# Kernel tuning notes

Hardware: AMD Instinct MI355X
Metric: run time of the kernel (lower is better)

Reference implementation:

```python
import jax, jax.numpy as jnp
import numpy as np

BATCH = 2048
N = 2 * BATCH
TEMP = 0.5
BN_EPS = 1e-5
COS_EPS = 1e-8

# Precompute (constant) flat indices of the negative entries: all (i,j) with
# j != i and j != i +- BATCH. Each row has exactly N-2 negatives.
_mask = np.ones((N, N), dtype=bool)
np.fill_diagonal(_mask, False)
for _i in range(BATCH):
    _mask[_i, BATCH + _i] = False
    _mask[BATCH + _i, _i] = False
NEG_IDX = np.nonzero(_mask.reshape(-1))[0]  # (N*(N-2),)


def _projector(h, W1, gamma, beta, W2, b2):
    # Linear (no bias) -> BatchNorm1d (training-mode batch stats) -> ReLU -> Linear
    x = h @ W1.T                                   # (B, latent)
    mu = jnp.mean(x, axis=0)
    var = jnp.mean(jnp.square(x - mu), axis=0)     # biased var, as torch BN
    x = (x - mu) * jax.lax.rsqrt(var + BN_EPS) * gamma + beta
    x = jax.nn.relu(x)
    return x @ W2.T + b2                           # (B, proj)


def setup_inputs() -> dict:
    key = jax.random.key(0)
    ks = jax.random.split(key, 4)
    latent, proj = 2048, 256
    return {
        "h_i": jax.random.normal(ks[0], (BATCH, latent), jnp.float32),
        "h_j": jax.random.normal(ks[1], (BATCH, latent), jnp.float32),
        "W1": jax.random.normal(ks[2], (latent, latent), jnp.float32) / np.sqrt(latent),
        "gamma": jnp.ones((latent,), jnp.float32),
        "beta": jnp.zeros((latent,), jnp.float32),
        "W2": jax.random.normal(ks[3], (proj, latent), jnp.float32) / np.sqrt(latent),
        "b2": jnp.zeros((proj,), jnp.float32),
    }


def reference(h_i, h_j, W1, gamma, beta, W2, b2):
    z_i = _projector(h_i, W1, gamma, beta, W2, b2)
    z_j = _projector(h_j, W1, gamma, beta, W2, b2)
    z = jnp.concatenate([z_i, z_j], axis=0)                      # (N, proj)
    # cosine similarity: normalize once, then a single GEMM
    zn = z / jnp.maximum(jnp.linalg.norm(z, axis=1, keepdims=True), COS_EPS)
    sim = (zn @ zn.T) / TEMP                                     # (N, N)
    sim_i_j = jnp.diagonal(sim, offset=BATCH)                    # (BATCH,)
    sim_j_i = jnp.diagonal(sim, offset=-BATCH)                   # (BATCH,)
    positives = jnp.concatenate([sim_i_j, sim_j_i])[:, None]     # (N, 1)
    negatives = sim.reshape(-1)[NEG_IDX].reshape(N, N - 2)       # (N, N-2)
    logits = jnp.concatenate([positives, negatives], axis=1)     # (N, N-1)
    # cross-entropy with label 0 for every row, reduction='sum', then / N
    loss = jnp.sum(jax.nn.logsumexp(logits, axis=1) - logits[:, 0]) / N
    return loss
```

## Files before the change

### kernel.cpp

```cpp
#include <hip/hip_runtime.h>
#include <hip/hip_fp8.h>
#include <math.h>

#define BATCH   2048
#define NROWS   4096
#define LATENT  2048
#define PROJ    256
#define TEMP_INV 2.0f
#define BN_EPS  1e-5f
#define COS_EPS 1e-8f
#define W1SCALE 32.0f
#define W1INV   (1.0f / 32.0f)

typedef __bf16 bf16x8 __attribute__((ext_vector_type(8)));
typedef float  f32x4  __attribute__((ext_vector_type(4)));
typedef long   i64;

__device__ __forceinline__ unsigned short f2bf(float f) {
    union { float f; unsigned int u; } c; c.f = f;
    return (unsigned short)((c.u + 0x7FFFu + ((c.u >> 16) & 1u)) >> 16);
}
__device__ __forceinline__ float bf2f(unsigned short h) {
    union { unsigned int u; float f; } c; c.u = ((unsigned int)h) << 16;
    return c.f;
}
__device__ __forceinline__ unsigned char f2fp8(float f) {
    __hip_fp8_e4m3 t(f);
    return (unsigned char)t.__x;
}

__device__ __forceinline__ void gl_lds16(const void* g, void* l) {
    __builtin_amdgcn_global_load_lds(
        (const __attribute__((address_space(1))) void*)g,
        (__attribute__((address_space(3))) void*)l, 16, 0, 0);
}

__device__ __forceinline__ int swz(int R, int lk) {
    return R * 32 + ((lk ^ ((R >> 1) & 3)) << 3);
}
__device__ __forceinline__ int mix8(int R) {
    return (R & 7) ^ ((R >> 1) & 4);
}

#define G1 1048576
#define G2 2097152
#define G3 3145728
#define G4 3276800
__global__ __launch_bounds__(256) void cvt_all_kernel(
    const float* __restrict__ h_i, const float* __restrict__ h_j,
    const float* __restrict__ W1,  const float* __restrict__ W2,
    unsigned char* __restrict__ Hq, unsigned char* __restrict__ W1q,
    unsigned short* __restrict__ W2b)
{
    int i = blockIdx.x * 256 + threadIdx.x;
    if (i >= G4) return;
    if (i < G2) {
        const float* src = (i < G1) ? h_i : h_j;
        int off = (i < G1) ? i : i - G1;
        float4 v = reinterpret_cast<const float4*>(src)[off];
        uchar4 o;
        o.x = f2fp8(v.x); o.y = f2fp8(v.y); o.z = f2fp8(v.z); o.w = f2fp8(v.w);
        reinterpret_cast<uchar4*>(Hq)[i] = o;
    } else if (i < G3) {
        int off = i - G2;
        float4 v = reinterpret_cast<const float4*>(W1)[off];
        uchar4 o;
        o.x = f2fp8(v.x * W1SCALE); o.y = f2fp8(v.y * W1SCALE);
        o.z = f2fp8(v.z * W1SCALE); o.w = f2fp8(v.w * W1SCALE);
        reinterpret_cast<uchar4*>(W1q)[off] = o;
    } else {
        int off = i - G3;
        float4 v = reinterpret_cast<const float4*>(W2)[off];
        ushort4 o;
        o.x = f2bf(v.x); o.y = f2bf(v.y); o.z = f2bf(v.z); o.w = f2bf(v.w);
        reinterpret_cast<ushort4*>(W2b)[off] = o;
    }
}

template<int KSTRIDE, int KLEN, int WM, int WN>
__device__ __forceinline__ void mfma_loop(
    const unsigned short* __restrict__ Ab,
    const unsigned short* __restrict__ Bb,
    unsigned short* As, unsigned short* Bs,
    f32x4 acc[WM][WN], int tid)
{
    constexpr int BM = WM * 32;
    constexpr int BN = WN * 32;
    const int wid = tid >> 6, lane = tid & 63;
    const int mblk = (wid >> 1) * (WM * 16);
    const int nblk = (wid & 1) * (WN * 16);
    const int lr = lane & 15, lk = lane >> 4;
    for (int k0 = 0; k0 < KLEN; k0 += 32) {
        __syncthreads();
        #pragma unroll
        for (int u = 0; u < BM / 64; ++u) {
            int li = u * 256 + tid;
            int r = li >> 2, c = (li & 3) ^ ((li >> 3) & 3);
            gl_lds16(Ab + (size_t)r * KSTRIDE + k0 + c * 8, As + li * 8);
        }
        #pragma unroll
        for (int u = 0; u < BN / 64; ++u) {
            int li = u * 256 + tid;
            int r = li >> 2, c = (li & 3) ^ ((li >> 3) & 3);
            gl_lds16(Bb + (size_t)r * KSTRIDE + k0 + c * 8, Bs + li * 8);
        }
        __syncthreads();
        bf16x8 af[WM], bv[WN];
        #pragma unroll
        for (int i = 0; i < WM; ++i)
            af[i] = *reinterpret_cast<const bf16x8*>(As + swz(mblk + i * 16 + lr, lk));
        #pragma unroll
        for (int j = 0; j < WN; ++j)
            bv[j] = *reinterpret_cast<const bf16x8*>(Bs + swz(nblk + j * 16 + lr, lk));
        #pragma unroll
        for (int i = 0; i < WM; ++i)
            #pragma unroll
            for (int j = 0; j < WN; ++j)
                acc[i][j] = __builtin_amdgcn_mfma_f32_16x16x32_bf16(af[i], bv[j], acc[i][j], 0, 0, 0);
    }
}

__global__ __launch_bounds__(256) void gemm1_fp8(
    const unsigned char* __restrict__ Hq, const unsigned char* __restrict__ W1q,
    unsigned short* __restrict__ Xb, float* __restrict__ sums, float* __restrict__ sumsqs)
{
    __shared__ __align__(16) unsigned char As[128 * 128];
    __shared__ __align__(16) unsigned char Bs[128 * 128];
    const int tid = threadIdx.x;
    const int m0 = blockIdx.y * 128, n0 = blockIdx.x * 128;
    const unsigned char* Ab = Hq + (size_t)m0 * LATENT;
    const unsigned char* Bb = W1q + (size_t)n0 * LATENT;
    const int wid = tid >> 6, lane = tid & 63;
    const int mblk = (wid >> 1) * 64, nblk = (wid & 1) * 64;
    const int lr = lane & 15, lk = lane >> 4;
    f32x4 zero = {0.f, 0.f, 0.f, 0.f};
    f32x4 acc[4][4];
    #pragma unroll
    for (int i = 0; i < 4; ++i)
        #pragma unroll
        for (int j = 0; j < 4; ++j) acc[i][j] = zero;

    for (int k0 = 0; k0 < LATENT; k0 += 128) {
        __syncthreads();
        #pragma unroll
        for (int u = 0; u < 4; ++u) {
            int li = u * 256 + tid;
            int r = li >> 3, s = li & 7;
            int c = s ^ mix8(r);
            gl_lds16(Ab + (size_t)r * LATENT + k0 + c * 16, As + li * 16);
        }
        #pragma unroll
        for (int u = 0; u < 4; ++u) {
            int li = u * 256 + tid;
            int r = li >> 3, s = li & 7;
            int c = s ^ mix8(r);
            gl_lds16(Bb + (size_t)r * LATENT + k0 + c * 16, Bs + li * 16);
        }
        __syncthreads();
        i64 af[4][4], bv[4][4];
        #pragma unroll
        for (int i = 0; i < 4; ++i) {
            int R = mblk + i * 16 + lr;
            int mr = mix8(R);
            int base = R * 128 + (lk & 1) * 8;
            #pragma unroll
            for (int t = 0; t < 4; ++t) {
                int g = 2 * t + (lk >> 1);
                af[i][t] = *reinterpret_cast<const i64*>(As + base + ((g ^ mr) << 4));
            }
        }
        #pragma unroll
        for (int j = 0; j < 4; ++j) {
            int R = nblk + j * 16 + lr;
            int mr = mix8(R);
            int base = R * 128 + (lk & 1) * 8;
            #pragma unroll
            for (int t = 0; t < 4; ++t) {
                int g = 2 * t + (lk >> 1);
                bv[j][t] = *reinterpret_cast<const i64*>(Bs + base + ((g ^ mr) << 4));
            }
        }
        #pragma unroll
        for (int t = 0; t < 4; ++t)
            #pragma unroll
            for (int i = 0; i < 4; ++i)
                #pragma unroll
                for (int j = 0; j < 4; ++j)
                    acc[i][j] = __builtin_amdgcn_mfma_f32_16x16x32_fp8_fp8(
                        af[i][t], bv[j][t], acc[i][j], 0, 0, 0);
    }

    const int lq = lane >> 4;
    const int half = m0 >> 11;
    #pragma unroll
    for (int j = 0; j < 4; ++j) {
        float s = 0.f, q = 0.f;
        #pragma unroll
        for (int i = 0; i < 4; ++i)
            #pragma unroll
            for (int r = 0; r < 4; ++r) {
                float v = acc[i][j][r] * W1INV;
                s += v; q += v * v;
                int row = m0 + mblk + i * 16 + lq * 4 + r;
                int col = n0 + nblk + j * 16 + lr;
                Xb[(size_t)row * LATENT + col] = f2bf(v);
            }
        s += __shfl_xor(s, 16, 64);  q += __shfl_xor(q, 16, 64);
        s += __shfl_xor(s, 32, 64);  q += __shfl_xor(q, 32, 64);
        if (lq == 0) {
            int col = n0 + nblk + j * 16 + lr;
            atomicAdd(&sums[half * LATENT + col], s);
            atomicAdd(&sumsqs[half * LATENT + col], q);
        }
    }
}

__global__ __launch_bounds__(256) void bn_final_kernel(
    const float* __restrict__ sums, const float* __restrict__ sumsqs,
    const float* __restrict__ gamma, const float* __restrict__ beta,
    float* __restrict__ scaleA, float* __restrict__ shiftA)
{
    const int idx = blockIdx.x * 256 + threadIdx.x;
    const int c = idx & (LATENT - 1);
    float mu  = sums[idx] * (1.0f / BATCH);
    float var = sumsqs[idx] * (1.0f / BATCH) - mu * mu;
    float inv = rsqrtf(var + BN_EPS);
    float sc = gamma[c] * inv;
    scaleA[idx] = sc;
    shiftA[idx] = beta[c] - mu * sc;
}

__global__ __launch_bounds__(256) void gemm2_mfma(
    const unsigned short* __restrict__ Xb, const unsigned short* __restrict__ W2b,
    const float* __restrict__ scaleA, const float* __restrict__ shiftA,
    float* __restrict__ Zp)
{
    __shared__ __align__(16) unsigned short As[128 * 32];
    __shared__ __align__(16) unsigned short Bs[64 * 32];
    const int tid = threadIdx.x;
    const int m0 = blockIdx.y * 128, n0 = blockIdx.x * 64, kc = blockIdx.z;
    const unsigned short* Ab = Xb + (size_t)m0 * LATENT + kc * 512;
    const unsigned short* Bb = W2b + (size_t)n0 * LATENT + kc * 512;
    const int half = m0 >> 11;
    const float* scp = scaleA + half * LATENT + kc * 512;
    const float* shp = shiftA + half * LATENT + kc * 512;
    const int wid = tid >> 6, lane = tid & 63;
    const int mblk = (wid >> 1) * 64, nblk = (wid & 1) * 32;
    const int lr = lane & 15, lk = lane >> 4;
    f32x4 zero = {0.f, 0.f, 0.f, 0.f};
    f32x4 acc[4][2];
    #pragma unroll
    for (int i = 0; i < 4; ++i) { acc[i][0] = zero; acc[i][1] = zero; }

    for (int k0 = 0; k0 < 512; k0 += 32) {
        __syncthreads();
        #pragma unroll
        for (int u = 0; u < 2; ++u) {
            int li = u * 256 + tid;
            int r = li >> 2, c = (li & 3) ^ ((li >> 3) & 3);
            gl_lds16(Ab + (size_t)r * LATENT + k0 + c * 8, As + li * 8);
        }
        {
            int li = tid;
            int r = li >> 2, c = (li & 3) ^ ((li >> 3) & 3);
            gl_lds16(Bb + (size_t)r * LATENT + k0 + c * 8, Bs + li * 8);
        }
        __syncthreads();
        float4 sc0 = *reinterpret_cast<const float4*>(scp + k0 + lk * 8);
        float4 sc1 = *reinterpret_cast<const float4*>(scp + k0 + lk * 8 + 4);
        float4 sh0 = *reinterpret_cast<const float4*>(shp + k0 + lk * 8);
        float4 sh1 = *reinterpret_cast<const float4*>(shp + k0 + lk * 8 + 4);
        bf16x8 af[4], bv[2];
        #pragma unroll
        for (int i = 0; i < 4; ++i) {
            bf16x8 raw = *reinterpret_cast<const bf16x8*>(As + swz(mblk + i * 16 + lr, lk));
            bf16x8 a;
            a[0] = (__bf16)fmaxf(fmaf((float)raw[0], sc0.x, sh0.x), 0.f);
            a[1] = (__bf16)fmaxf(fmaf((float)raw[1], sc0.y, sh0.y), 0.f);
            a[2] = (__bf16)fmaxf(fmaf((float)raw[2], sc0.z, sh0.z), 0.f);
            a[3] = (__bf16)fmaxf(fmaf((float)raw[3], sc0.w, sh0.w), 0.f);
            a[4] = (__bf16)fmaxf(fmaf((float)raw[4], sc1.x, sh1.x), 0.f);
            a[5] = (__bf16)fmaxf(fmaf((float)raw[5], sc1.y, sh1.y), 0.f);
            a[6] = (__bf16)fmaxf(fmaf((float)raw[6], sc1.z, sh1.z), 0.f);
            a[7] = (__bf16)fmaxf(fmaf((float)raw[7], sc1.w, sh1.w), 0.f);
            af[i] = a;
        }
        #pragma unroll
        for (int j = 0; j < 2; ++j)
            bv[j] = *reinterpret_cast<const bf16x8*>(Bs + swz(nblk + j * 16 + lr, lk));
        #pragma unroll
        for (int i = 0; i < 4; ++i)
            #pragma unroll
            for (int j = 0; j < 2; ++j)
                acc[i][j] = __builtin_amdgcn_mfma_f32_16x16x32_bf16(af[i], bv[j], acc[i][j], 0, 0, 0);
    }

    float* Zk = Zp + (size_t)kc * NROWS * PROJ;
    const int lq = lane >> 4;
    #pragma unroll
    for (int i = 0; i < 4; ++i)
        #pragma unroll
        for (int j = 0; j < 2; ++j)
            #pragma unroll
            for (int r = 0; r < 4; ++r) {
                int row = m0 + mblk + i * 16 + lq * 4 + r;
                int col = n0 + nblk + j * 16 + lr;
                Zk[(size_t)row * PROJ + col] = acc[i][j][r];
            }
}

__global__ __launch_bounds__(256) void rownorm_kernel(
    const float* __restrict__ Zp, const float* __restrict__ b2,
    unsigned short* __restrict__ ZNb)
{
    const int wave = threadIdx.x >> 6;
    const int lane = threadIdx.x & 63;
    const int row = blockIdx.x * 4 + wave;
    float v[4];
    float sq = 0.f;
    #pragma unroll
    for (int i = 0; i < 4; ++i) {
        int col = lane + i * 64;
        float t = b2[col];
        #pragma unroll
        for (int c = 0; c < 4; ++c)
            t += Zp[(size_t)c * NROWS * PROJ + (size_t)row * PROJ + col];
        v[i] = t;
        sq += t * t;
    }
    #pragma unroll
    for (int off = 32; off > 0; off >>= 1) sq += __shfl_xor(sq, off, 64);
    float inv = 1.0f / fmaxf(sqrtf(sq), COS_EPS);
    #pragma unroll
    for (int i = 0; i < 4; ++i)
        ZNb[(size_t)row * PROJ + lane + i * 64] = f2bf(v[i] * inv);
}

__global__ __launch_bounds__(256) void simlse_mfma(
    const unsigned short* __restrict__ ZNb, float* __restrict__ rowsum,
    float* __restrict__ dgA, float* __restrict__ posA)
{
    if (blockIdx.x < blockIdx.y) return;
    __shared__ __align__(16) unsigned short As[128 * 32];
    __shared__ __align__(16) unsigned short Bs[128 * 32];
    const int tid = threadIdx.x;
    const int r0 = blockIdx.y * 128, j0 = blockIdx.x * 128;
    const bool offdiag = (j0 != r0);
    f32x4 zero = {0.f, 0.f, 0.f, 0.f};
    f32x4 acc[4][4];
    #pragma unroll
    for (int i = 0; i < 4; ++i)
        #pragma unroll
        for (int j = 0; j < 4; ++j) acc[i][j] = zero;
    mfma_loop<PROJ, PROJ, 4, 4>(ZNb + (size_t)r0 * PROJ, ZNb + (size_t)j0 * PROJ,
                                As, Bs, acc, tid);
    const int wid = tid >> 6, lane = tid & 63;
    const int mblk = (wid >> 1) * 64, nblk = (wid & 1) * 64;
    const int lr = lane & 15, lq = lane >> 4;
    float tcol[4] = {0.f, 0.f, 0.f, 0.f};
    #pragma unroll
    for (int i = 0; i < 4; ++i)
        #pragma unroll
        for (int r = 0; r < 4; ++r) {
            int R = r0 + mblk + i * 16 + lq * 4 + r;
            int P = (R < BATCH) ? R + BATCH : R - BATCH;
            float t = 0.f;
            #pragma unroll
            for (int j = 0; j < 4; ++j) {
                int J = j0 + nblk + j * 16 + lr;
                float s = acc[i][j][r] * TEMP_INV;
                float e = __expf(s);
                t += e;
                tcol[j] += e;
                if (J == R) dgA[R] = e;
                if (J == P) { posA[R] = s; posA[J] = s; }
            }
            t += __shfl_xor(t, 1, 64);
            t += __shfl_xor(t, 2, 64);
            t += __shfl_xor(t, 4, 64);
            t += __shfl_xor(t, 8, 64);
            if (lr == 0) atomicAdd(&rowsum[R], t);
        }
    if (offdiag) {
        #pragma unroll
        for (int j = 0; j < 4; ++j) {
            float c = tcol[j];
            c += __shfl_xor(c, 16, 64);
            c += __shfl_xor(c, 32, 64);
            if (lq == 0) atomicAdd(&rowsum[j0 + nblk + j * 16 + lr], c);
        }
    }
}

__global__ __launch_bounds__(256) void loss_kernel(
    const float* __restrict__ rowsum, const float* __restrict__ dgA,
    const float* __restrict__ posA, float* __restrict__ out)
{
    __shared__ float red[256];
    float s = 0.f;
    for (int r = threadIdx.x; r < NROWS; r += 256)
        s += logf(rowsum[r] - dgA[r]) - posA[r];
    red[threadIdx.x] = s;
    __syncthreads();
    for (int off = 128; off > 0; off >>= 1) {
        if (threadIdx.x < off) red[threadIdx.x] += red[threadIdx.x + off];
        __syncthreads();
    }
    if (threadIdx.x == 0) out[0] = red[0] * (1.0f / NROWS);
}

extern "C" void kernel_launch(void* const* d_in, const int* in_sizes, int n_in,
                              void* d_out, int out_size, void* d_ws, size_t ws_size,
                              hipStream_t stream)
{
    const float* h_i   = (const float*)d_in[0];
    const float* h_j   = (const float*)d_in[1];
    const float* W1    = (const float*)d_in[2];
    const float* gamma = (const float*)d_in[3];
    const float* beta  = (const float*)d_in[4];
    const float* W2    = (const float*)d_in[5];
    const float* b2    = (const float*)d_in[6];
    float* out = (float*)d_out;

    float* Zp     = (float*)d_ws;
    float* sums   = Zp + (size_t)4 * NROWS * PROJ;
    float* sumsqs = sums + 2 * LATENT;
    float* rowsum = sumsqs + 2 * LATENT;
    float* scaleA = rowsum + NROWS;
    float* shiftA = scaleA + 2 * LATENT;
    float* dgA    = shiftA + 2 * LATENT;
    float* posA   = dgA + NROWS;
    unsigned char* Hq  = (unsigned char*)(posA + NROWS);
    unsigned char* W1q = Hq + (size_t)NROWS * LATENT;
    unsigned short* W2b = (unsigned short*)(W1q + (size_t)LATENT * LATENT);
    unsigned short* Xb  = W2b + (size_t)PROJ * LATENT;
    unsigned short* ZNb = Xb + (size_t)NROWS * LATENT;

    hipMemsetAsync(sums, 0, (size_t)(4 * LATENT + NROWS) * sizeof(float), stream);

    cvt_all_kernel<<<(G4 + 255) / 256, 256, 0, stream>>>(h_i, h_j, W1, W2, Hq, W1q, W2b);
    gemm1_fp8<<<dim3(LATENT / 128, NROWS / 128), 256, 0, stream>>>(Hq, W1q, Xb, sums, sumsqs);
    bn_final_kernel<<<(2 * LATENT) / 256, 256, 0, stream>>>(sums, sumsqs, gamma, beta, scaleA, shiftA);
    gemm2_mfma<<<dim3(PROJ / 64, NROWS / 128, 4), 256, 0, stream>>>(Xb, W2b, scaleA, shiftA, Zp);
    rownorm_kernel<<<NROWS / 4, 256, 0, stream>>>(Zp, b2, ZNb);
    simlse_mfma<<<dim3(NROWS / 128, NROWS / 128), 256, 0, stream>>>(ZNb, rowsum, dgA, posA);
    loss_kernel<<<1, 256, 0, stream>>>(rowsum, dgA, posA, out);
}
```

Measured before the change: 185.4 us.

## Shrink gemm1 tile, fuse BN finalize into gemm2, store split-K partials as bf16

Three changes land together. The FP8 projector GEMM now uses a 128x64 tile with an occupancy hint, which doubles the grid to 1024 blocks and halves the accumulator registers. The separate BN finalize kernel is removed: each gemm2 block recomputes scale and shift for its K-slice into shared memory, which saves a launch at the cost of some redundant work. The split-K partial outputs are written as bf16 instead of fp32, halving that traffic but adding rounding error before the row normalization.

```diff
diff --git a/kernel.cpp b/kernel.cpp
--- a/kernel.cpp
+++ b/kernel.cpp
@@ -120,25 +120,23 @@
     }
 }
 
-__global__ __launch_bounds__(256) void gemm1_fp8(
+__global__ __launch_bounds__(256, 4) void gemm1_fp8(
     const unsigned char* __restrict__ Hq, const unsigned char* __restrict__ W1q,
     unsigned short* __restrict__ Xb, float* __restrict__ sums, float* __restrict__ sumsqs)
 {
     __shared__ __align__(16) unsigned char As[128 * 128];
-    __shared__ __align__(16) unsigned char Bs[128 * 128];
+    __shared__ __align__(16) unsigned char Bs[64 * 128];
     const int tid = threadIdx.x;
-    const int m0 = blockIdx.y * 128, n0 = blockIdx.x * 128;
+    const int m0 = blockIdx.y * 128, n0 = blockIdx.x * 64;
     const unsigned char* Ab = Hq + (size_t)m0 * LATENT;
     const unsigned char* Bb = W1q + (size_t)n0 * LATENT;
     const int wid = tid >> 6, lane = tid & 63;
-    const int mblk = (wid >> 1) * 64, nblk = (wid & 1) * 64;
+    const int mblk = (wid >> 1) * 64, nblk = (wid & 1) * 32;
     const int lr = lane & 15, lk = lane >> 4;
     f32x4 zero = {0.f, 0.f, 0.f, 0.f};
-    f32x4 acc[4][4];
-    #pragma unroll
-    for (int i = 0; i < 4; ++i)
-        #pragma unroll
-        for (int j = 0; j < 4; ++j) acc[i][j] = zero;
+    f32x4 acc[4][2];
+    #pragma unroll
+    for (int i = 0; i < 4; ++i) { acc[i][0] = zero; acc[i][1] = zero; }
 
     for (int k0 = 0; k0 < LATENT; k0 += 128) {
         __syncthreads();
@@ -146,18 +144,16 @@
         for (int u = 0; u < 4; ++u) {
             int li = u * 256 + tid;
             int r = li >> 3, s = li & 7;
-            int c = s ^ mix8(r);
-            gl_lds16(Ab + (size_t)r * LATENT + k0 + c * 16, As + li * 16);
-        }
-        #pragma unroll
-        for (int u = 0; u < 4; ++u) {
+            gl_lds16(Ab + (size_t)r * LATENT + k0 + ((s ^ mix8(r)) * 16), As + li * 16);
+        }
+        #pragma unroll
+        for (int u = 0; u < 2; ++u) {
             int li = u * 256 + tid;
             int r = li >> 3, s = li & 7;
-            int c = s ^ mix8(r);
-            gl_lds16(Bb + (size_t)r * LATENT + k0 + c * 16, Bs + li * 16);
-        }
-        __syncthreads();
-        i64 af[4][4], bv[4][4];
+            gl_lds16(Bb + (size_t)r * LATENT + k0 + ((s ^ mix8(r)) * 16), Bs + li * 16);
+        }
+        __syncthreads();
+        i64 af[4][4], bv[2][4];
         #pragma unroll
         for (int i = 0; i < 4; ++i) {
             int R = mblk + i * 16 + lr;
@@ -170,7 +166,7 @@
             }
         }
         #pragma unroll
-        for (int j = 0; j < 4; ++j) {
+        for (int j = 0; j < 2; ++j) {
             int R = nblk + j * 16 + lr;
             int mr = mix8(R);
             int base = R * 128 + (lk & 1) * 8;
@@ -185,7 +181,7 @@
             #pragma unroll
             for (int i = 0; i < 4; ++i)
                 #pragma unroll
-                for (int j = 0; j < 4; ++j)
+                for (int j = 0; j < 2; ++j)
                     acc[i][j] = __builtin_amdgcn_mfma_f32_16x16x32_fp8_fp8(
                         af[i][t], bv[j][t], acc[i][j], 0, 0, 0);
     }
@@ -193,7 +189,7 @@
     const int lq = lane >> 4;
     const int half = m0 >> 11;
     #pragma unroll
-    for (int j = 0; j < 4; ++j) {
+    for (int j = 0; j < 2; ++j) {
         float s = 0.f, q = 0.f;
         #pragma unroll
         for (int i = 0; i < 4; ++i)
@@ -215,35 +211,32 @@
     }
 }
 
-__global__ __launch_bounds__(256) void bn_final_kernel(
+__global__ __launch_bounds__(256) void gemm2_mfma(
+    const unsigned short* __restrict__ Xb, const unsigned short* __restrict__ W2b,
     const float* __restrict__ sums, const float* __restrict__ sumsqs,
     const float* __restrict__ gamma, const float* __restrict__ beta,
-    float* __restrict__ scaleA, float* __restrict__ shiftA)
-{
-    const int idx = blockIdx.x * 256 + threadIdx.x;
-    const int c = idx & (LATENT - 1);
-    float mu  = sums[idx] * (1.0f / BATCH);
-    float var = sumsqs[idx] * (1.0f / BATCH) - mu * mu;
-    float inv = rsqrtf(var + BN_EPS);
-    float sc = gamma[c] * inv;
-    scaleA[idx] = sc;
-    shiftA[idx] = beta[c] - mu * sc;
-}
-
-__global__ __launch_bounds__(256) void gemm2_mfma(
-    const unsigned short* __restrict__ Xb, const unsigned short* __restrict__ W2b,
-    const float* __restrict__ scaleA, const float* __restrict__ shiftA,
-    float* __restrict__ Zp)
+    unsigned short* __restrict__ Zpb)
 {
     __shared__ __align__(16) unsigned short As[128 * 32];
     __shared__ __align__(16) unsigned short Bs[64 * 32];
+    __shared__ __align__(16) float scs[512];
+    __shared__ __align__(16) float shs[512];
     const int tid = threadIdx.x;
     const int m0 = blockIdx.y * 128, n0 = blockIdx.x * 64, kc = blockIdx.z;
     const unsigned short* Ab = Xb + (size_t)m0 * LATENT + kc * 512;
     const unsigned short* Bb = W2b + (size_t)n0 * LATENT + kc * 512;
     const int half = m0 >> 11;
-    const float* scp = scaleA + half * LATENT + kc * 512;
-    const float* shp = shiftA + half * LATENT + kc * 512;
+    #pragma unroll
+    for (int u = 0; u < 2; ++u) {
+        int e = u * 256 + tid;
+        int col = kc * 512 + e;
+        int g = half * LATENT + col;
+        float mu  = sums[g] * (1.0f / BATCH);
+        float var = sumsqs[g] * (1.0f / BATCH) - mu * mu;
+        float sc = gamma[col] * rsqrtf(var + BN_EPS);
+        scs[e] = sc;
+        shs[e] = beta[col] - mu * sc;
+    }
     const int wid = tid >> 6, lane = tid & 63;
     const int mblk = (wid >> 1) * 64, nblk = (wid & 1) * 32;
     const int lr = lane & 15, lk = lane >> 4;
@@ -266,10 +259,10 @@
             gl_lds16(Bb + (size_t)r * LATENT + k0 + c * 8, Bs + li * 8);
         }
         __syncthreads();
-        float4 sc0 = *reinterpret_cast<const float4*>(scp + k0 + lk * 8);
-        float4 sc1 = *reinterpret_cast<const float4*>(scp + k0 + lk * 8 + 4);
-        float4 sh0 = *reinterpret_cast<const float4*>(shp + k0 + lk * 8);
-        float4 sh1 = *reinterpret_cast<const float4*>(shp + k0 + lk * 8 + 4);
+        float4 sc0 = *reinterpret_cast<const float4*>(scs + k0 + lk * 8);
+        float4 sc1 = *reinterpret_cast<const float4*>(scs + k0 + lk * 8 + 4);
+        float4 sh0 = *reinterpret_cast<const float4*>(shs + k0 + lk * 8);
+        float4 sh1 = *reinterpret_cast<const float4*>(shs + k0 + lk * 8 + 4);
         bf16x8 af[4], bv[2];
         #pragma unroll
         for (int i = 0; i < 4; ++i) {
@@ -295,7 +288,7 @@
                 acc[i][j] = __builtin_amdgcn_mfma_f32_16x16x32_bf16(af[i], bv[j], acc[i][j], 0, 0, 0);
     }
 
-    float* Zk = Zp + (size_t)kc * NROWS * PROJ;
+    unsigned short* Zk = Zpb + (size_t)kc * NROWS * PROJ;
     const int lq = lane >> 4;
     #pragma unroll
     for (int i = 0; i < 4; ++i)
@@ -305,12 +298,12 @@
             for (int r = 0; r < 4; ++r) {
                 int row = m0 + mblk + i * 16 + lq * 4 + r;
                 int col = n0 + nblk + j * 16 + lr;
-                Zk[(size_t)row * PROJ + col] = acc[i][j][r];
+                Zk[(size_t)row * PROJ + col] = f2bf(acc[i][j][r]);
             }
 }
 
 __global__ __launch_bounds__(256) void rownorm_kernel(
-    const float* __restrict__ Zp, const float* __restrict__ b2,
+    const unsigned short* __restrict__ Zpb, const float* __restrict__ b2,
     unsigned short* __restrict__ ZNb)
 {
     const int wave = threadIdx.x >> 6;
@@ -324,7 +317,7 @@
         float t = b2[col];
         #pragma unroll
         for (int c = 0; c < 4; ++c)
-            t += Zp[(size_t)c * NROWS * PROJ + (size_t)row * PROJ + col];
+            t += bf2f(Zpb[(size_t)c * NROWS * PROJ + (size_t)row * PROJ + col]);
         v[i] = t;
         sq += t * t;
     }
@@ -422,13 +415,11 @@
     const float* b2    = (const float*)d_in[6];
     float* out = (float*)d_out;
 
-    float* Zp     = (float*)d_ws;
-    float* sums   = Zp + (size_t)4 * NROWS * PROJ;
+    unsigned short* Zpb = (unsigned short*)d_ws;
+    float* sums   = (float*)(Zpb + (size_t)4 * NROWS * PROJ);
     float* sumsqs = sums + 2 * LATENT;
     float* rowsum = sumsqs + 2 * LATENT;
-    float* scaleA = rowsum + NROWS;
-    float* shiftA = scaleA + 2 * LATENT;
-    float* dgA    = shiftA + 2 * LATENT;
+    float* dgA    = rowsum + NROWS;
     float* posA   = dgA + NROWS;
     unsigned char* Hq  = (unsigned char*)(posA + NROWS);
     unsigned char* W1q = Hq + (size_t)NROWS * LATENT;
@@ -439,10 +430,9 @@
     hipMemsetAsync(sums, 0, (size_t)(4 * LATENT + NROWS) * sizeof(float), stream);
 
     cvt_all_kernel<<<(G4 + 255) / 256, 256, 0, stream>>>(h_i, h_j, W1, W2, Hq, W1q, W2b);
-    gemm1_fp8<<<dim3(LATENT / 128, NROWS / 128), 256, 0, stream>>>(Hq, W1q, Xb, sums, sumsqs);
-    bn_final_kernel<<<(2 * LATENT) / 256, 256, 0, stream>>>(sums, sumsqs, gamma, beta, scaleA, shiftA);
-    gemm2_mfma<<<dim3(PROJ / 64, NROWS / 128, 4), 256, 0, stream>>>(Xb, W2b, scaleA, shiftA, Zp);
-    rownorm_kernel<<<NROWS / 4, 256, 0, stream>>>(Zp, b2, ZNb);
+    gemm1_fp8<<<dim3(LATENT / 64, NROWS / 128), 256, 0, stream>>>(Hq, W1q, Xb, sums, sumsqs);
+    gemm2_mfma<<<dim3(PROJ / 64, NROWS / 128, 4), 256, 0, stream>>>(Xb, W2b, sums, sumsqs, gamma, beta, Zpb);
+    rownorm_kernel<<<NROWS / 4, 256, 0, stream>>>(Zpb, b2, ZNb);
     simlse_mfma<<<dim3(NROWS / 128, NROWS / 128), 256, 0, stream>>>(ZNb, rowsum, dgA, posA);
     loss_kernel<<<1, 256, 0, stream>>>(rowsum, dgA, posA, out);
 }
```

New measurement: 176.0 us. -5.1%, faster.
